# Performance work log

Hardware: AMD Instinct MI355X
Metric: run time of the kernel (lower is better)

## Reference

```python
import jax, jax.numpy as jnp
from jax import lax
import numpy as np

B, V, T, K, HE, TH, E, L = 128, 30000, 50, 50, 256, 800, 300, 3
DELTA = 0.005


def setup_inputs() -> dict:
    key = jax.random.key(0)
    ks = jax.random.split(key, 24)
    rn = lambda k, s, sc=0.05: jax.random.normal(k, s, jnp.float32) * sc
    return dict(
        X=jax.random.uniform(ks[0], (B, V), jnp.float32),
        timestamp=jax.random.randint(ks[1], (B,), 0, T),
        X_mean=jax.random.uniform(ks[2], (T, V), jnp.float32),
        W_eta_map=rn(ks[3], (HE, V)), b_eta_map=rn(ks[4], (HE,)),
        lstm_Wih=rn(ks[5], (L, 4 * HE, HE)), lstm_Whh=rn(ks[6], (L, 4 * HE, HE)),
        lstm_bih=rn(ks[7], (L, 4 * HE)), lstm_bhh=rn(ks[8], (L, 4 * HE)),
        W_qeta_mu=rn(ks[9], (K, HE + K)), b_qeta_mu=rn(ks[10], (K,)),
        W_qeta_ls=rn(ks[11], (K, HE + K)), b_qeta_ls=rn(ks[12], (K,)),
        W1=rn(ks[13], (TH, V + K)), b1=rn(ks[14], (TH,)),
        W2=rn(ks[15], (TH, TH)), b2=rn(ks[16], (TH,)),
        W_qt_mu=rn(ks[17], (K, TH)), b_qt_mu=rn(ks[18], (K,)),
        W_qt_ls=rn(ks[19], (K, TH)), b_qt_ls=rn(ks[20], (K,)),
        mu_q_alpha=rn(ks[21], (K, T, E), 0.1),
        logsigma_q_alpha=rn(ks[22], (K, T, E), 0.1),
        emb=rn(ks[23], (V, E), 0.1),
    )


def _lstm(x, Wih, Whh, bih, bhh):
    # PyTorch-style multi-layer LSTM, batch=1 squeezed away; x: [T, HE]
    for l in range(Wih.shape[0]):
        Wi, Wh, bi, bh = Wih[l], Whh[l], bih[l], bhh[l]
        def step(carry, xt, Wi=Wi, Wh=Wh, bi=bi, bh=bh):
            h, c = carry
            g = Wi @ xt + Wh @ h + bi + bh
            i, f, gg, o = jnp.split(g, 4)  # torch gate order i,f,g,o
            c = jax.nn.sigmoid(f) * c + jax.nn.sigmoid(i) * jnp.tanh(gg)
            h = jax.nn.sigmoid(o) * jnp.tanh(c)
            return (h, c), h
        H = Wh.shape[1]
        _, x = lax.scan(step, (jnp.zeros(H, x.dtype), jnp.zeros(H, x.dtype)), x)
    return x


def reference(X, timestamp, X_mean, W_eta_map, b_eta_map, lstm_Wih, lstm_Whh,
              lstm_bih, lstm_bhh, W_qeta_mu, b_qeta_mu, W_qeta_ls, b_qeta_ls,
              W1, b1, W2, b2, W_qt_mu, b_qt_mu, W_qt_ls, b_qt_ls,
              mu_q_alpha, logsigma_q_alpha, emb):
    # eval-mode DETM forward (reparameterize returns mu when not training)
    nb = X / X.sum(1, keepdims=True)
    logd = jnp.log(jnp.float32(DELTA))
    Tn = X_mean.shape[0]
    first = jnp.arange(Tn) == 0

    # --- eta: LSTM over time then sequential Gaussian recurrence ---
    rnn_out = _lstm(X_mean @ W_eta_map.T + b_eta_map, lstm_Wih, lstm_Whh, lstm_bih, lstm_bhh)  # [T,HE]
    Kn = W_qeta_mu.shape[0]

    def eta_step(eta_prev, xs):
        out_t, f = xs
        h = jnp.concatenate([out_t, eta_prev])
        mu = W_qeta_mu @ h + b_qeta_mu
        ls = W_qeta_ls @ h + b_qeta_ls
        p_ls = jnp.where(f, 0.0, logd)  # prior: N(0,I) at t=0, N(eta_{t-1}, delta) after
        kl = 0.5 * jnp.sum((jnp.exp(ls) + (mu - eta_prev) ** 2) / (jnp.exp(p_ls) + 1e-6) - 1.0 + p_ls - ls)
        return mu, (mu, kl)  # eval: eta_t = mu_t

    _, (etas, kls_eta) = lax.scan(eta_step, jnp.zeros(Kn, X.dtype), (rnn_out, first))
    kl_eta = kls_eta.sum()

    # --- theta ---
    eta_td = etas[timestamp]  # [B,K]
    h = jnp.tanh(jnp.concatenate([nb, eta_td], axis=1) @ W1.T + b1)
    h = jnp.tanh(h @ W2.T + b2)
    mu_t = h @ W_qt_mu.T + b_qt_mu
    ls_t = h @ W_qt_ls.T + b_qt_ls
    theta = jax.nn.softmax(mu_t, axis=-1)  # eval: z = mu
    kl_theta = (0.5 * jnp.sum((jnp.exp(ls_t) + (mu_t - eta_td) ** 2) / (1.0 + 1e-6) - 1.0 - ls_t, axis=-1)).sum()

    # --- alpha (eval: alpha_t = mu_q_alpha[:,t,:]) ---
    alphas = jnp.transpose(mu_q_alpha, (1, 0, 2))      # [T,K,E]
    q_ls = jnp.transpose(logsigma_q_alpha, (1, 0, 2))
    p_mu = jnp.concatenate([jnp.zeros_like(alphas[:1]), alphas[:-1]], axis=0)
    p_ls = jnp.where(first[:, None, None], 0.0, logd)
    kl_alpha = (0.5 * jnp.sum((jnp.exp(q_ls) + (alphas - p_mu) ** 2) / (jnp.exp(p_ls) + 1e-6) - 1.0 + p_ls - q_ls, axis=-1)).sum()

    # --- beta, likelihood ---
    beta = jax.nn.softmax(jnp.einsum('tke,ve->tkv', alphas, emb), axis=-1)  # [T,K,V]
    px = jnp.einsum('bk,bkv->bv', theta, beta[timestamp])
    lnpx = jnp.log(px + 1e-6)
    nll = (-lnpx * X).sum(-1).mean()
    return theta, lnpx, beta, nll, kl_alpha, kl_eta, kl_theta
```

## Files before the change

### kernel.cpp

```cpp
#include <hip/hip_runtime.h>
#include <math.h>

#define B_  128
#define V_  30000
#define T_  50
#define K_  50
#define HE_ 256
#define TH_ 800
#define E_  300
#define L_  3

#define LOGD_ (-5.2983173665480363f)

typedef short bf16x8 __attribute__((ext_vector_type(8)));
typedef float f32x4  __attribute__((ext_vector_type(4)));

#define TM 64
#define TN 64
#define TK 16

__global__ __launch_bounds__(256) void gemm_nt(
    const float* __restrict__ A, int lda, int M,
    const float* __restrict__ B, int ldb, int N,
    int K,
    float* __restrict__ C, int ldc,
    const float* __restrict__ bias, int mode, int kchunk)
{
    __shared__ float As[TK][TM + 4];
    __shared__ float Bs[TK][TN + 4];
    const int tid = threadIdx.x;
    const int bm = blockIdx.y * TM;
    const int bn = blockIdx.x * TN;
    const int tx = tid & 15;
    const int ty = tid >> 4;
    const int lr = tid >> 2;
    const int lc = (tid & 3) << 2;

    float acc[4][4];
#pragma unroll
    for (int i = 0; i < 4; ++i)
#pragma unroll
        for (int j = 0; j < 4; ++j) acc[i][j] = 0.f;

    const int kbeg = blockIdx.z * kchunk;
    const int kend = min(K, kbeg + kchunk);

    for (int k0 = kbeg; k0 < kend; k0 += TK) {
        {
            float v0 = 0.f, v1 = 0.f, v2 = 0.f, v3 = 0.f;
            int gr = bm + lr;
            if (gr < M) {
                const float* p = A + (size_t)gr * lda + k0 + lc;
                int rem = K - (k0 + lc);
                if (rem >= 4) {
                    float2 a0 = *(const float2*)p;
                    float2 a1 = *(const float2*)(p + 2);
                    v0 = a0.x; v1 = a0.y; v2 = a1.x; v3 = a1.y;
                } else {
                    if (rem > 0) v0 = p[0];
                    if (rem > 1) v1 = p[1];
                    if (rem > 2) v2 = p[2];
                }
            }
            As[lc + 0][lr] = v0; As[lc + 1][lr] = v1;
            As[lc + 2][lr] = v2; As[lc + 3][lr] = v3;
        }
        {
            float v0 = 0.f, v1 = 0.f, v2 = 0.f, v3 = 0.f;
            int gr = bn + lr;
            if (gr < N) {
                const float* p = B + (size_t)gr * ldb + k0 + lc;
                int rem = K - (k0 + lc);
                if (rem >= 4) {
                    float2 a0 = *(const float2*)p;
                    float2 a1 = *(const float2*)(p + 2);
                    v0 = a0.x; v1 = a0.y; v2 = a1.x; v3 = a1.y;
                } else {
                    if (rem > 0) v0 = p[0];
                    if (rem > 1) v1 = p[1];
                    if (rem > 2) v2 = p[2];
                }
            }
            Bs[lc + 0][lr] = v0; Bs[lc + 1][lr] = v1;
            Bs[lc + 2][lr] = v2; Bs[lc + 3][lr] = v3;
        }
        __syncthreads();
#pragma unroll
        for (int kk = 0; kk < TK; ++kk) {
            float a[4], b[4];
#pragma unroll
            for (int i = 0; i < 4; ++i) a[i] = As[kk][ty * 4 + i];
#pragma unroll
            for (int j = 0; j < 4; ++j) b[j] = Bs[kk][tx * 4 + j];
#pragma unroll
            for (int i = 0; i < 4; ++i)
#pragma unroll
                for (int j = 0; j < 4; ++j) acc[i][j] += a[i] * b[j];
        }
        __syncthreads();
    }

#pragma unroll
    for (int i = 0; i < 4; ++i) {
        int row = bm + ty * 4 + i;
        if (row >= M) continue;
#pragma unroll
        for (int j = 0; j < 4; ++j) {
            int col = bn + tx * 4 + j;
            if (col >= N) continue;
            float v = acc[i][j];
            if (mode == 3) {
                atomicAdd(&C[(size_t)row * ldc + col], v);
            } else {
                if (mode == 1) v = tanhf(v + bias[col]);
                else if (mode == 2) v = v + bias[col];
                C[(size_t)row * ldc + col] = v;
            }
        }
    }
}

__global__ __launch_bounds__(256) void bias_act(
    float* __restrict__ C, const float* __restrict__ bias,
    int total, int N, int mode)
{
    int idx = blockIdx.x * 256 + threadIdx.x;
    if (idx >= total) return;
    int j = idx % N;
    float v = C[idx] + bias[j];
    if (mode == 1) v = tanhf(v);
    C[idx] = v;
}

__global__ __launch_bounds__(256) void rowsum_inv(const float* __restrict__ X,
                                                  float* __restrict__ inv)
{
    int b = blockIdx.x;
    const float4* p = (const float4*)(X + (size_t)b * V_);
    float s = 0.f;
    for (int i = threadIdx.x; i < V_ / 4; i += 256) {
        float4 v = p[i];
        s += v.x + v.y + v.z + v.w;
    }
    for (int off = 32; off; off >>= 1) s += __shfl_down(s, off);
    __shared__ float red[4];
    int wid = threadIdx.x >> 6, lane = threadIdx.x & 63;
    if (lane == 0) red[wid] = s;
    __syncthreads();
    if (threadIdx.x == 0) inv[b] = 1.f / (red[0] + red[1] + red[2] + red[3]);
}

#define NLB 32

__global__ __launch_bounds__(256) void lstm_all(
    const float* __restrict__ rnn_in,
    const float* __restrict__ Wih,
    const float* __restrict__ Whh,
    const float* __restrict__ bih,
    const float* __restrict__ bhh,
    float* __restrict__ houtA,
    float* __restrict__ houtB,
    float* __restrict__ houtF,
    float* __restrict__ hping,
    int* __restrict__ barcnt)
{
    __shared__ float sx[8 * 36];
    __shared__ float sh[8 * 36];
    __shared__ float sg[32];
    const int tid = threadIdx.x;
    const int blk = blockIdx.x;
    const int row_local = tid >> 3;
    const int chunk = tid & 7;
    const int gate = row_local >> 3;
    const int jloc = row_local & 7;
    const int gr = gate * HE_ + blk * 8 + jloc;
    const int seg = tid >> 5, sidx = tid & 31;

    for (int l = 0; l < L_; ++l) {
        float4 wih[8], whh[8];
        const float4* pi = (const float4*)(Wih + ((size_t)l * 4 * HE_ + gr) * HE_ + chunk * 32);
        const float4* pw = (const float4*)(Whh + ((size_t)l * 4 * HE_ + gr) * HE_ + chunk * 32);
#pragma unroll
        for (int q = 0; q < 8; ++q) { wih[q] = pi[q]; whh[q] = pw[q]; }
        const float bias = bih[l * 4 * HE_ + gr] + bhh[l * 4 * HE_ + gr];
        const float* xs = (l == 0) ? rnn_in : ((l == 1) ? houtA : houtB);
        float* hd = (l == 0) ? houtA : ((l == 1) ? houtB : houtF);
        float cst = 0.f;

        for (int t = 0; t < T_; ++t) {
            const int wb = t & 1, rb = wb ^ 1;
            float xv = xs[t * HE_ + tid];
            float hv = (t > 0) ? hping[rb * HE_ + tid] : 0.f;
            sx[seg * 36 + sidx] = xv;
            sh[seg * 36 + sidx] = hv;
            __syncthreads();

            float acc = 0.f;
#pragma unroll
            for (int q = 0; q < 8; ++q) {
                float4 a = *(const float4*)&sx[chunk * 36 + q * 4];
                float4 b = *(const float4*)&sh[chunk * 36 + q * 4];
                float4 wa = wih[q], wc = whh[q];
                acc += wa.x * a.x + wa.y * a.y + wa.z * a.z + wa.w * a.w
                     + wc.x * b.x + wc.y * b.y + wc.z * b.z + wc.w * b.w;
            }
            acc += __shfl_xor(acc, 1);
            acc += __shfl_xor(acc, 2);
            acc += __shfl_xor(acc, 4);
            if (chunk == 0) sg[row_local] = acc + bias;
            __syncthreads();

            if (tid < 8) {
                float gi = sg[tid], gf = sg[8 + tid], gg = sg[16 + tid], go = sg[24 + tid];
                float si = 1.f / (1.f + expf(-gi));
                float sf = 1.f / (1.f + expf(-gf));
                float so = 1.f / (1.f + expf(-go));
                cst = sf * cst + si * tanhf(gg);
                float hn = so * tanhf(cst);
                int j = blk * 8 + tid;
                hping[wb * HE_ + j] = hn;
                hd[t * HE_ + j] = hn;
            }

            if (tid < 64) __threadfence();
            __syncthreads();
            if (tid == 0) {
                __hip_atomic_fetch_add(barcnt, 1, __ATOMIC_ACQ_REL, __HIP_MEMORY_SCOPE_AGENT);
                const int tgt = (l * T_ + t + 1) * NLB;
                while (__hip_atomic_load(barcnt, __ATOMIC_ACQUIRE, __HIP_MEMORY_SCOPE_AGENT) < tgt)
                    __builtin_amdgcn_s_sleep(1);
            }
            __syncthreads();
        }
    }
}

__global__ __launch_bounds__(256) void eta_scan(
    const float* __restrict__ rnn_out,
    const float* __restrict__ Wmu, const float* __restrict__ bmu,
    const float* __restrict__ Wls, const float* __restrict__ bls,
    float* __restrict__ etas,
    float* __restrict__ kl_eta_out)
{
    __shared__ float hbuf[HE_ + K_];
    __shared__ float smu[K_];
    __shared__ float red[256];
    const int tid = threadIdx.x;
    const int k = tid >> 2, c = tid & 3;
    if (tid < K_) hbuf[HE_ + tid] = 0.f;
    float kl = 0.f;
    __syncthreads();
    for (int t = 0; t < T_; ++t) {
        if (tid < HE_) hbuf[tid] = rnn_out[t * HE_ + tid];
        __syncthreads();
        if (k < K_) {
            const float* wm = Wmu + k * (HE_ + K_);
            const float* wl = Wls + k * (HE_ + K_);
            float am = 0.f, al = 0.f;
            for (int i = c; i < HE_ + K_; i += 4) {
                float hv = hbuf[i];
                am += wm[i] * hv;
                al += wl[i] * hv;
            }
            am += __shfl_xor(am, 1); am += __shfl_xor(am, 2);
            al += __shfl_xor(al, 1); al += __shfl_xor(al, 2);
            if (c == 0) {
                float mu = am + bmu[k];
                float ls = al + bls[k];
                float eprev = hbuf[HE_ + k];
                float pls = (t == 0) ? 0.f : LOGD_;
                float d = mu - eprev;
                kl += 0.5f * ((expf(ls) + d * d) / (expf(pls) + 1e-6f) - 1.f + pls - ls);
                etas[t * K_ + k] = mu;
                smu[k] = mu;
            }
        }
        __syncthreads();
        if (tid < K_) hbuf[HE_ + tid] = smu[tid];
        __syncthreads();
    }
    red[tid] = kl;
    __syncthreads();
    if (tid == 0) {
        float s = 0.f;
        for (int i = 0; i < 256; ++i) s += red[i];
        *kl_eta_out = s;
    }
}

__global__ __launch_bounds__(256) void h1_epilogue(
    const float* __restrict__ C1, const float* __restrict__ inv,
    const float* __restrict__ etas, const int* __restrict__ ts,
    const float* __restrict__ W1, const float* __restrict__ b1,
    float* __restrict__ h1)
{
    int idx = blockIdx.x * 256 + threadIdx.x;
    if (idx >= B_ * TH_) return;
    int b = idx / TH_, j = idx % TH_;
    const float* e = etas + ts[b] * K_;
    const float* w = W1 + (size_t)j * (V_ + K_) + V_;
    float s = 0.f;
#pragma unroll
    for (int k = 0; k < K_; ++k) s += e[k] * w[k];
    h1[idx] = tanhf(C1[idx] * inv[b] + s + b1[j]);
}

__global__ __launch_bounds__(64) void theta_kernel(
    const float* __restrict__ mu_t, const float* __restrict__ ls_t,
    const float* __restrict__ etas, const int* __restrict__ ts,
    float* __restrict__ theta, float* __restrict__ kl_out)
{
    int b = blockIdx.x;
    int lane = threadIdx.x;
    bool ok = lane < K_;
    float m = ok ? mu_t[b * K_ + lane] : -3.4e38f;
    float mx = m;
    for (int off = 32; off; off >>= 1) mx = fmaxf(mx, __shfl_down(mx, off));
    mx = __shfl(mx, 0);
    float e = ok ? expf(m - mx) : 0.f;
    float s = e;
    for (int off = 32; off; off >>= 1) s += __shfl_down(s, off);
    s = __shfl(s, 0);
    if (ok) theta[b * K_ + lane] = e / s;
    float kl = 0.f;
    if (ok) {
        float ls = ls_t[b * K_ + lane];
        float d = m - etas[ts[b] * K_ + lane];
        kl = 0.5f * ((expf(ls) + d * d) / (1.f + 1e-6f) - 1.f - ls);
    }
    for (int off = 32; off; off >>= 1) kl += __shfl_down(kl, off);
    if (lane == 0) atomicAdd(kl_out, kl);
}

#define KP_   320
#define MPAD_ 2560
#define NPAD_ 30080

__global__ __launch_bounds__(256) void conv_alpha(
    const float* __restrict__ mu, short* __restrict__ Ah, short* __restrict__ Al)
{
    int idx = blockIdx.x * 256 + threadIdx.x;
    if (idx >= MPAD_ * KP_) return;
    int row = idx / KP_, e = idx % KP_;
    float v = 0.f;
    if (row < T_ * K_ && e < E_) {
        int t = row / K_, k = row % K_;
        v = mu[((size_t)k * T_ + t) * E_ + e];
    }
    unsigned int u = __float_as_uint(v);
    Ah[idx] = (short)(u >> 16);
    float hf = __uint_as_float(u & 0xFFFF0000u);
    Al[idx] = (short)(__float_as_uint(v - hf) >> 16);
}

__global__ __launch_bounds__(512, 4) void gemm_beta(
    const short* __restrict__ Ah, const short* __restrict__ Al,
    const float* __restrict__ Bf,
    float* __restrict__ Cexp,
    float* __restrict__ bsum)
{
    __shared__ __align__(16) short lds[4 * 8192];
    const int tid = threadIdx.x;
    const int lane = tid & 63;
    const int w = tid >> 6;
    const int wr = w >> 2, wc = w & 3;
    const int l15 = lane & 15, l4 = lane >> 4;

    const int NM = MPAD_ / 128;
    const int nwg = (NPAD_ / 128) * NM;
    const int qq_ = nwg / 8, rr_ = nwg % 8;
    int orig = blockIdx.x;
    int xcd = orig & 7, ixc = orig >> 3;
    int wg = (xcd < rr_ ? xcd * (qq_ + 1) : rr_ * (qq_ + 1) + (xcd - rr_) * qq_) + ixc;
    const int bn = (wg / NM) * 128;
    const int bm = (wg % NM) * 128;

    f32x4 acc[4][2];
#pragma unroll
    for (int mi = 0; mi < 4; ++mi)
#pragma unroll
        for (int ni = 0; ni < 2; ++ni) acc[mi][ni] = (f32x4){0.f, 0.f, 0.f, 0.f};

    uint4  va[4];
    float4 vb[4];

    auto loadTile = [&](int k0) {
#pragma unroll
        for (int q = 0; q < 4; ++q) {
            int L = q * 512 + tid;
            int tile = L >> 10;
            int c = L & 1023;
            int r = c >> 3;
            int k8 = (c & 7) ^ (r & 7);
            const short* src = (tile ? Al : Ah) + (size_t)(bm + r) * KP_ + k0 + k8 * 8;
            va[q] = *(const uint4*)src;
        }
#pragma unroll
        for (int q = 0; q < 2; ++q) {
            int L = q * 512 + tid;
            int r = L >> 3;
            int k8 = (L & 7) ^ (r & 7);
            int rg = bn + r;
            int kb = k0 + k8 * 8;
            float4 u0, u1;
            if (rg < V_ && kb + 8 <= E_) {
                u0 = *(const float4*)(Bf + (size_t)rg * E_ + kb);
                u1 = *(const float4*)(Bf + (size_t)rg * E_ + kb + 4);
            } else {
                float t[8];
#pragma unroll
                for (int e = 0; e < 8; ++e) {
                    int kk = kb + e;
                    t[e] = (rg < V_ && kk < E_) ? Bf[(size_t)rg * E_ + kk] : 0.f;
                }
                u0.x = t[0]; u0.y = t[1]; u0.z = t[2]; u0.w = t[3];
                u1.x = t[4]; u1.y = t[5]; u1.z = t[6]; u1.w = t[7];
            }
            vb[q * 2] = u0; vb[q * 2 + 1] = u1;
        }
    };
    auto writeTile = [&]() {
#pragma unroll
        for (int q = 0; q < 4; ++q) {
            int L = q * 512 + tid;
            int tile = L >> 10;
            int c = L & 1023;
            *(uint4*)&lds[(size_t)(tile * 1024 + c) * 8] = va[q];
        }
#pragma unroll
        for (int q = 0; q < 2; ++q) {
            int L = q * 512 + tid;
            float vv[8];
            float4 u0 = vb[q * 2], u1 = vb[q * 2 + 1];
            vv[0] = u0.x; vv[1] = u0.y; vv[2] = u0.z; vv[3] = u0.w;
            vv[4] = u1.x; vv[5] = u1.y; vv[6] = u1.z; vv[7] = u1.w;
            unsigned int hpk[4], lpk[4];
#pragma unroll
            for (int e = 0; e < 8; e += 2) {
                unsigned int b0 = __float_as_uint(vv[e]);
                unsigned int b1 = __float_as_uint(vv[e + 1]);
                hpk[e >> 1] = (b0 >> 16) | (b1 & 0xFFFF0000u);
                float d0 = vv[e]     - __uint_as_float(b0 & 0xFFFF0000u);
                float d1 = vv[e + 1] - __uint_as_float(b1 & 0xFFFF0000u);
                lpk[e >> 1] = (__float_as_uint(d0) >> 16) | (__float_as_uint(d1) & 0xFFFF0000u);
            }
            uint4 hv; hv.x = hpk[0]; hv.y = hpk[1]; hv.z = hpk[2]; hv.w = hpk[3];
            uint4 lv; lv.x = lpk[0]; lv.y = lpk[1]; lv.z = lpk[2]; lv.w = lpk[3];
            *(uint4*)&lds[(size_t)(2048 + L) * 8] = hv;
            *(uint4*)&lds[(size_t)(3072 + L) * 8] = lv;
        }
    };

    loadTile(0);
    writeTile();
    __syncthreads();

    for (int k0 = 0; k0 < KP_; k0 += 64) {
        const bool nxt = (k0 + 64) < KP_;
        if (nxt) loadTile(k0 + 64);

#pragma unroll
        for (int ks = 0; ks < 2; ++ks) {
            bf16x8 fbh[2], fbl[2];
#pragma unroll
            for (int ni = 0; ni < 2; ++ni) {
                int r = wc * 32 + ni * 16 + l15;
                int s = r * 8 + ((ks * 4 + l4) ^ (r & 7));
                fbh[ni] = *(const bf16x8*)&lds[(size_t)(2048 + s) * 8];
                fbl[ni] = *(const bf16x8*)&lds[(size_t)(3072 + s) * 8];
            }
#pragma unroll
            for (int mi = 0; mi < 4; ++mi) {
                int r = wr * 64 + mi * 16 + l15;
                int s = r * 8 + ((ks * 4 + l4) ^ (r & 7));
                bf16x8 fah = *(const bf16x8*)&lds[(size_t)s * 8];
                bf16x8 fal = *(const bf16x8*)&lds[(size_t)(1024 + s) * 8];
#pragma unroll
                for (int ni = 0; ni < 2; ++ni) {
                    acc[mi][ni] = __builtin_amdgcn_mfma_f32_16x16x32_bf16(
                        fah, fbh[ni], acc[mi][ni], 0, 0, 0);
                    acc[mi][ni] = __builtin_amdgcn_mfma_f32_16x16x32_bf16(
                        fah, fbl[ni], acc[mi][ni], 0, 0, 0);
                    acc[mi][ni] = __builtin_amdgcn_mfma_f32_16x16x32_bf16(
                        fal, fbh[ni], acc[mi][ni], 0, 0, 0);
                }
            }
        }
        __syncthreads();
        if (nxt) {
            writeTile();
            __syncthreads();
        }
    }

#pragma unroll
    for (int mi = 0; mi < 4; ++mi) {
#pragma unroll
        for (int reg = 0; reg < 4; ++reg) {
            int grow = bm + wr * 64 + mi * 16 + (l4 << 2) + reg;
            float rs = 0.f;
            float ex[2];
#pragma unroll
            for (int ni = 0; ni < 2; ++ni) {
                int gcol = bn + wc * 32 + ni * 16 + l15;
                float e = (gcol < V_) ? __expf(acc[mi][ni][reg]) : 0.f;
                ex[ni] = e;
                rs += e;
            }
            if (grow < T_ * K_) {
#pragma unroll
                for (int ni = 0; ni < 2; ++ni) {
                    int gcol = bn + wc * 32 + ni * 16 + l15;
                    if (gcol < V_) Cexp[(size_t)grow * V_ + gcol] = ex[ni];
                }
            }
            rs += __shfl_xor(rs, 1);
            rs += __shfl_xor(rs, 2);
            rs += __shfl_xor(rs, 4);
            rs += __shfl_xor(rs, 8);
            if (l15 == 0 && grow < T_ * K_) atomicAdd(&bsum[grow], rs);
        }
    }
}

__global__ __launch_bounds__(256) void beta_scale(
    float* __restrict__ beta, const float* __restrict__ bsum)
{
    const int total4 = T_ * K_ * (V_ / 4);
    for (int i = blockIdx.x * 256 + threadIdx.x; i < total4; i += gridDim.x * 256) {
        int row = i / (V_ / 4);
        float inv = 1.f / bsum[row];
        float4 v = ((const float4*)beta)[i];
        v.x *= inv; v.y *= inv; v.z *= inv; v.w *= inv;
        ((float4*)beta)[i] = v;
    }
}

__global__ __launch_bounds__(256) void px_kernel(
    const float* __restrict__ beta, const float* __restrict__ theta,
    const int* __restrict__ ts, const float* __restrict__ X,
    float* __restrict__ lnpx, float* __restrict__ nll_acc)
{
    __shared__ float sb[K_][256];
    int t = blockIdx.y;
    int tid = threadIdx.x;
    int v = blockIdx.x * 256 + tid;
    bool vok = v < V_;
    bool any = false;
    for (int b = 0; b < B_; ++b) any |= (ts[b] == t);
    if (!any) return;
    for (int k = 0; k < K_; ++k)
        sb[k][tid] = vok ? beta[((size_t)t * K_ + k) * V_ + v] : 0.f;
    __syncthreads();
    float acc = 0.f;
    for (int b = 0; b < B_; ++b) {
        if (ts[b] != t) continue;
        const float* th = theta + b * K_;
        float px = 0.f;
#pragma unroll
        for (int k = 0; k < K_; ++k) px += th[k] * sb[k][tid];
        float l = logf(px + 1e-6f);
        if (vok) {
            lnpx[(size_t)b * V_ + v] = l;
            acc += l * X[(size_t)b * V_ + v];
        }
    }
    for (int off = 32; off; off >>= 1) acc += __shfl_down(acc, off);
    __shared__ float red[4];
    int wid = tid >> 6, lane = tid & 63;
    if (lane == 0) red[wid] = acc;
    __syncthreads();
    if (tid == 0) atomicAdd(nll_acc, red[0] + red[1] + red[2] + red[3]);
}

__global__ __launch_bounds__(256) void kl_alpha_kernel(
    const float* __restrict__ mu, const float* __restrict__ lsig,
    float* __restrict__ out)
{
    int idx = blockIdx.x * 256 + threadIdx.x;
    float term = 0.f;
    if (idx < K_ * T_ * E_) {
        int r = idx % (T_ * E_);
        int t = r / E_;
        float a = mu[idx];
        float q = lsig[idx];
        float pmu = (t > 0) ? mu[idx - E_] : 0.f;
        float pls = (t > 0) ? LOGD_ : 0.f;
        float d = a - pmu;
        term = 0.5f * ((expf(q) + d * d) / (expf(pls) + 1e-6f) - 1.f + pls - q);
    }
    for (int off = 32; off; off >>= 1) term += __shfl_down(term, off);
    __shared__ float red[4];
    int wid = threadIdx.x >> 6, lane = threadIdx.x & 63;
    if (lane == 0) red[wid] = term;
    __syncthreads();
    if (threadIdx.x == 0) atomicAdd(out, red[0] + red[1] + red[2] + red[3]);
}

__global__ void finalize_nll(const float* __restrict__ acc, float* __restrict__ out)
{
    *out = -acc[0] * (1.f / (float)B_);
}

extern "C" void kernel_launch(void* const* d_in, const int* in_sizes, int n_in,
                              void* d_out, int out_size, void* d_ws, size_t ws_size,
                              hipStream_t stream)
{
    const float* X          = (const float*)d_in[0];
    const int*   ts         = (const int*)d_in[1];
    const float* X_mean     = (const float*)d_in[2];
    const float* W_eta_map  = (const float*)d_in[3];
    const float* b_eta_map  = (const float*)d_in[4];
    const float* lstm_Wih   = (const float*)d_in[5];
    const float* lstm_Whh   = (const float*)d_in[6];
    const float* lstm_bih   = (const float*)d_in[7];
    const float* lstm_bhh   = (const float*)d_in[8];
    const float* W_qeta_mu  = (const float*)d_in[9];
    const float* b_qeta_mu  = (const float*)d_in[10];
    const float* W_qeta_ls  = (const float*)d_in[11];
    const float* b_qeta_ls  = (const float*)d_in[12];
    const float* W1         = (const float*)d_in[13];
    const float* b1         = (const float*)d_in[14];
    const float* W2         = (const float*)d_in[15];
    const float* b2         = (const float*)d_in[16];
    const float* W_qt_mu    = (const float*)d_in[17];
    const float* b_qt_mu    = (const float*)d_in[18];
    const float* W_qt_ls    = (const float*)d_in[19];
    const float* b_qt_ls    = (const float*)d_in[20];
    const float* mu_q_alpha = (const float*)d_in[21];
    const float* ls_q_alpha = (const float*)d_in[22];
    const float* emb        = (const float*)d_in[23];

    float* out     = (float*)d_out;
    float* o_theta = out;
    float* o_lnpx  = out + (size_t)B_ * K_;
    float* o_beta  = o_lnpx + (size_t)B_ * V_;
    float* o_scal  = o_beta + (size_t)T_ * K_ * V_;

    float* ws = (float*)d_ws;
    float* w_inv   = ws;
    float* w_rnn   = ws + 128;
    float* w_seq0  = ws + 12928;
    float* w_houtA = ws + 38528;
    float* w_houtB = ws + 51328;
    float* w_hping = ws + 64128;
    float* w_barc  = ws + 64640;
    float* w_etas  = ws + 89728;
    float* w_h1    = ws + 92228;
    float* w_h2    = ws + 194628;
    float* w_mu    = ws + 297028;
    float* w_ls    = ws + 303428;
    float* w_nll   = ws + 309828;
    float* w_bsum  = ws + 309832;
    short* w_Ah    = (short*)(ws + 312344);
    short* w_Al    = (short*)(ws + 721944);

    hipMemsetAsync(o_scal, 0, 4 * sizeof(float), stream);
    hipMemsetAsync(w_h1, 0, (size_t)(102400 + 102400 + 6400 + 6400 + 1) * sizeof(float), stream);
    hipMemsetAsync(w_rnn, 0, (size_t)T_ * HE_ * sizeof(float), stream);
    hipMemsetAsync(w_barc, 0, sizeof(int), stream);
    hipMemsetAsync(w_bsum, 0, (size_t)T_ * K_ * sizeof(float), stream);

    rowsum_inv<<<B_, 256, 0, stream>>>(X, w_inv);

    gemm_nt<<<dim3(HE_ / TN, 1, 125), 256, 0, stream>>>(
        X_mean, V_, T_, W_eta_map, V_, HE_, V_, w_rnn, HE_, nullptr, 3, 240);
    bias_act<<<(T_ * HE_ + 255) / 256, 256, 0, stream>>>(
        w_rnn, b_eta_map, T_ * HE_, HE_, 2);

    lstm_all<<<NLB, 256, 0, stream>>>(
        w_rnn, lstm_Wih, lstm_Whh, lstm_bih, lstm_bhh,
        w_houtA, w_houtB, w_seq0, w_hping, (int*)w_barc);

    eta_scan<<<1, 256, 0, stream>>>(w_seq0, W_qeta_mu, b_qeta_mu,
                                    W_qeta_ls, b_qeta_ls, w_etas, o_scal + 2);

    gemm_nt<<<dim3((TH_ + TN - 1) / TN, (B_ + TM - 1) / TM, 75), 256, 0, stream>>>(
        X, V_, B_, W1, V_ + K_, TH_, V_, w_h1, TH_, nullptr, 3, 400);
    h1_epilogue<<<(B_ * TH_ + 255) / 256, 256, 0, stream>>>(
        w_h1, w_inv, w_etas, ts, W1, b1, w_h1);

    gemm_nt<<<dim3((TH_ + TN - 1) / TN, (B_ + TM - 1) / TM, 10), 256, 0, stream>>>(
        w_h1, TH_, B_, W2, TH_, TH_, TH_, w_h2, TH_, nullptr, 3, 80);
    bias_act<<<(B_ * TH_ + 255) / 256, 256, 0, stream>>>(
        w_h2, b2, B_ * TH_, TH_, 1);

    gemm_nt<<<dim3(1, (B_ + TM - 1) / TM, 25), 256, 0, stream>>>(
        w_h2, TH_, B_, W_qt_mu, TH_, K_, TH_, w_mu, K_, nullptr, 3, 32);
    gemm_nt<<<dim3(1, (B_ + TM - 1) / TM, 25), 256, 0, stream>>>(
        w_h2, TH_, B_, W_qt_ls, TH_, K_, TH_, w_ls, K_, nullptr, 3, 32);
    bias_act<<<(B_ * K_ + 255) / 256, 256, 0, stream>>>(
        w_mu, b_qt_mu, B_ * K_, K_, 2);
    bias_act<<<(B_ * K_ + 255) / 256, 256, 0, stream>>>(
        w_ls, b_qt_ls, B_ * K_, K_, 2);

    theta_kernel<<<B_, 64, 0, stream>>>(w_mu, w_ls, w_etas, ts, o_theta, o_scal + 3);

    conv_alpha<<<(MPAD_ * KP_ + 255) / 256, 256, 0, stream>>>(mu_q_alpha, w_Ah, w_Al);
    gemm_beta<<<(NPAD_ / 128) * (MPAD_ / 128), 512, 0, stream>>>(
        w_Ah, w_Al, emb, o_beta, w_bsum);
    beta_scale<<<2048, 256, 0, stream>>>(o_beta, w_bsum);

    px_kernel<<<dim3((V_ + 255) / 256, T_), 256, 0, stream>>>(
        o_beta, o_theta, ts, X, o_lnpx, w_nll);

    kl_alpha_kernel<<<(K_ * T_ * E_ + 255) / 256, 256, 0, stream>>>(
        mu_q_alpha, ls_q_alpha, o_scal + 1);

    finalize_nll<<<1, 1, 0, stream>>>(w_nll, o_scal);
}
```

Baseline: 2.572 ms.

## Use split-bf16 MFMA GEMM for large reductions and pipeline LSTM layers

Adds a bf16x3 MFMA GEMM that splits each fp32 operand into high and low bf16 parts, with a swizzled LDS layout and register prefetch. It replaces the scalar fp32 GEMM for the two large V-length reductions (X_mean·W_eta and X·W1). The LSTM is restructured so each of the three layers runs on its own 16-block group, pipelined over time through per-layer counters instead of one global barrier per step. The trade-offs are slightly lower precision from the 3-term bf16 approximation and reliance on all 48 blocks being co-resident for the spin waits.

```diff
diff --git a/kernel.cpp b/kernel.cpp
--- a/kernel.cpp
+++ b/kernel.cpp
@@ -120,6 +120,144 @@
     }
 }
 
+__global__ __launch_bounds__(512, 4) void gemm_bf3(
+    const float* __restrict__ A, int lda, int M,
+    const float* __restrict__ B, int ldb, int N,
+    int K,
+    float* __restrict__ C, int ldc, int kchunk)
+{
+    __shared__ __align__(16) short lds[4 * 8192];
+    const int tid = threadIdx.x;
+    const int lane = tid & 63;
+    const int w = tid >> 6;
+    const int wr = w >> 2, wc = w & 3;
+    const int l15 = lane & 15, l4 = lane >> 4;
+    const int bm = blockIdx.y * 128;
+    const int bn = blockIdx.x * 128;
+    const int kbeg = blockIdx.z * kchunk;
+    const int kend = kbeg + kchunk;
+
+    f32x4 acc[4][2];
+#pragma unroll
+    for (int mi = 0; mi < 4; ++mi)
+#pragma unroll
+        for (int ni = 0; ni < 2; ++ni) acc[mi][ni] = (f32x4){0.f, 0.f, 0.f, 0.f};
+
+    float4 va[4], vb[4];
+
+    auto loadSide = [&](const float* __restrict__ P, int ldp, int Rlim,
+                        int base, int k0, float4* dst) {
+#pragma unroll
+        for (int q = 0; q < 2; ++q) {
+            int L = q * 512 + tid;
+            int r = L >> 3;
+            int k8 = (L & 7) ^ (r & 7);
+            int rg = base + r;
+            int kb = k0 + k8 * 8;
+            float4 u0, u1;
+            if (rg < Rlim && kb + 8 <= K) {
+                u0 = *(const float4*)(P + (size_t)rg * ldp + kb);
+                u1 = *(const float4*)(P + (size_t)rg * ldp + kb + 4);
+            } else {
+                float tt[8];
+#pragma unroll
+                for (int e = 0; e < 8; ++e) {
+                    int kk = kb + e;
+                    tt[e] = (rg < Rlim && kk < K) ? P[(size_t)rg * ldp + kk] : 0.f;
+                }
+                u0.x = tt[0]; u0.y = tt[1]; u0.z = tt[2]; u0.w = tt[3];
+                u1.x = tt[4]; u1.y = tt[5]; u1.z = tt[6]; u1.w = tt[7];
+            }
+            dst[q * 2] = u0; dst[q * 2 + 1] = u1;
+        }
+    };
+    auto writeSide = [&](const float4* src, int tbase) {
+#pragma unroll
+        for (int q = 0; q < 2; ++q) {
+            int L = q * 512 + tid;
+            float vv[8];
+            float4 u0 = src[q * 2], u1 = src[q * 2 + 1];
+            vv[0] = u0.x; vv[1] = u0.y; vv[2] = u0.z; vv[3] = u0.w;
+            vv[4] = u1.x; vv[5] = u1.y; vv[6] = u1.z; vv[7] = u1.w;
+            unsigned int hpk[4], lpk[4];
+#pragma unroll
+            for (int e = 0; e < 8; e += 2) {
+                unsigned int b0 = __float_as_uint(vv[e]);
+                unsigned int b1 = __float_as_uint(vv[e + 1]);
+                hpk[e >> 1] = (b0 >> 16) | (b1 & 0xFFFF0000u);
+                float d0 = vv[e]     - __uint_as_float(b0 & 0xFFFF0000u);
+                float d1 = vv[e + 1] - __uint_as_float(b1 & 0xFFFF0000u);
+                lpk[e >> 1] = (__float_as_uint(d0) >> 16) | (__float_as_uint(d1) & 0xFFFF0000u);
+            }
+            uint4 hv; hv.x = hpk[0]; hv.y = hpk[1]; hv.z = hpk[2]; hv.w = hpk[3];
+            uint4 lv; lv.x = lpk[0]; lv.y = lpk[1]; lv.z = lpk[2]; lv.w = lpk[3];
+            *(uint4*)&lds[(size_t)(tbase + L) * 8] = hv;
+            *(uint4*)&lds[(size_t)(tbase + 1024 + L) * 8] = lv;
+        }
+    };
+
+    loadSide(A, lda, M, bm, kbeg, va);
+    loadSide(B, ldb, N, bn, kbeg, vb);
+    writeSide(va, 0);
+    writeSide(vb, 2048);
+    __syncthreads();
+
+    for (int k0 = kbeg; k0 < kend; k0 += 64) {
+        const bool nxt = (k0 + 64) < kend;
+        if (nxt) {
+            loadSide(A, lda, M, bm, k0 + 64, va);
+            loadSide(B, ldb, N, bn, k0 + 64, vb);
+        }
+#pragma unroll
+        for (int ks = 0; ks < 2; ++ks) {
+            bf16x8 fbh[2], fbl[2];
+#pragma unroll
+            for (int ni = 0; ni < 2; ++ni) {
+                int r = wc * 32 + ni * 16 + l15;
+                int s = r * 8 + ((ks * 4 + l4) ^ (r & 7));
+                fbh[ni] = *(const bf16x8*)&lds[(size_t)(2048 + s) * 8];
+                fbl[ni] = *(const bf16x8*)&lds[(size_t)(3072 + s) * 8];
+            }
+#pragma unroll
+            for (int mi = 0; mi < 4; ++mi) {
+                int r = wr * 64 + mi * 16 + l15;
+                int s = r * 8 + ((ks * 4 + l4) ^ (r & 7));
+                bf16x8 fah = *(const bf16x8*)&lds[(size_t)s * 8];
+                bf16x8 fal = *(const bf16x8*)&lds[(size_t)(1024 + s) * 8];
+#pragma unroll
+                for (int ni = 0; ni < 2; ++ni) {
+                    acc[mi][ni] = __builtin_amdgcn_mfma_f32_16x16x32_bf16(
+                        fah, fbh[ni], acc[mi][ni], 0, 0, 0);
+                    acc[mi][ni] = __builtin_amdgcn_mfma_f32_16x16x32_bf16(
+                        fah, fbl[ni], acc[mi][ni], 0, 0, 0);
+                    acc[mi][ni] = __builtin_amdgcn_mfma_f32_16x16x32_bf16(
+                        fal, fbh[ni], acc[mi][ni], 0, 0, 0);
+                }
+            }
+        }
+        __syncthreads();
+        if (nxt) {
+            writeSide(va, 0);
+            writeSide(vb, 2048);
+            __syncthreads();
+        }
+    }
+
+#pragma unroll
+    for (int mi = 0; mi < 4; ++mi) {
+#pragma unroll
+        for (int reg = 0; reg < 4; ++reg) {
+            int grow = bm + wr * 64 + mi * 16 + (l4 << 2) + reg;
+            if (grow >= M) continue;
+#pragma unroll
+            for (int ni = 0; ni < 2; ++ni) {
+                int gcol = bn + wc * 32 + ni * 16 + l15;
+                if (gcol < N) atomicAdd(&C[(size_t)grow * ldc + gcol], acc[mi][ni][reg]);
+            }
+        }
+    }
+}
+
 __global__ __launch_bounds__(256) void bias_act(
     float* __restrict__ C, const float* __restrict__ bias,
     int total, int N, int mode)
@@ -150,9 +288,9 @@
     if (threadIdx.x == 0) inv[b] = 1.f / (red[0] + red[1] + red[2] + red[3]);
 }
 
-#define NLB 32
-
-__global__ __launch_bounds__(256) void lstm_all(
+#define GLB 16
+
+__global__ __launch_bounds__(256, 1) void lstm_pipe(
     const float* __restrict__ rnn_in,
     const float* __restrict__ Wih,
     const float* __restrict__ Whh,
@@ -161,77 +299,81 @@
     float* __restrict__ houtA,
     float* __restrict__ houtB,
     float* __restrict__ houtF,
-    float* __restrict__ hping,
-    int* __restrict__ barcnt)
-{
-    __shared__ float sx[8 * 36];
-    __shared__ float sh[8 * 36];
-    __shared__ float sg[32];
+    int* __restrict__ cnts)
+{
+    __shared__ __align__(16) float sx[HE_];
+    __shared__ __align__(16) float sh[HE_];
+    __shared__ float sg[64];
     const int tid = threadIdx.x;
-    const int blk = blockIdx.x;
-    const int row_local = tid >> 3;
-    const int chunk = tid & 7;
-    const int gate = row_local >> 3;
-    const int jloc = row_local & 7;
-    const int gr = gate * HE_ + blk * 8 + jloc;
-    const int seg = tid >> 5, sidx = tid & 31;
-
-    for (int l = 0; l < L_; ++l) {
-        float4 wih[8], whh[8];
-        const float4* pi = (const float4*)(Wih + ((size_t)l * 4 * HE_ + gr) * HE_ + chunk * 32);
-        const float4* pw = (const float4*)(Whh + ((size_t)l * 4 * HE_ + gr) * HE_ + chunk * 32);
-#pragma unroll
-        for (int q = 0; q < 8; ++q) { wih[q] = pi[q]; whh[q] = pw[q]; }
-        const float bias = bih[l * 4 * HE_ + gr] + bhh[l * 4 * HE_ + gr];
-        const float* xs = (l == 0) ? rnn_in : ((l == 1) ? houtA : houtB);
-        float* hd = (l == 0) ? houtA : ((l == 1) ? houtB : houtF);
-        float cst = 0.f;
-
-        for (int t = 0; t < T_; ++t) {
-            const int wb = t & 1, rb = wb ^ 1;
-            float xv = xs[t * HE_ + tid];
-            float hv = (t > 0) ? hping[rb * HE_ + tid] : 0.f;
-            sx[seg * 36 + sidx] = xv;
-            sh[seg * 36 + sidx] = hv;
-            __syncthreads();
-
-            float acc = 0.f;
-#pragma unroll
-            for (int q = 0; q < 8; ++q) {
-                float4 a = *(const float4*)&sx[chunk * 36 + q * 4];
-                float4 b = *(const float4*)&sh[chunk * 36 + q * 4];
-                float4 wa = wih[q], wc = whh[q];
-                acc += wa.x * a.x + wa.y * a.y + wa.z * a.z + wa.w * a.w
-                     + wc.x * b.x + wc.y * b.y + wc.z * b.z + wc.w * b.w;
-            }
-            acc += __shfl_xor(acc, 1);
-            acc += __shfl_xor(acc, 2);
-            acc += __shfl_xor(acc, 4);
-            if (chunk == 0) sg[row_local] = acc + bias;
-            __syncthreads();
-
-            if (tid < 8) {
-                float gi = sg[tid], gf = sg[8 + tid], gg = sg[16 + tid], go = sg[24 + tid];
-                float si = 1.f / (1.f + expf(-gi));
-                float sf = 1.f / (1.f + expf(-gf));
-                float so = 1.f / (1.f + expf(-go));
-                cst = sf * cst + si * tanhf(gg);
-                float hn = so * tanhf(cst);
-                int j = blk * 8 + tid;
-                hping[wb * HE_ + j] = hn;
-                hd[t * HE_ + j] = hn;
-            }
-
-            if (tid < 64) __threadfence();
-            __syncthreads();
-            if (tid == 0) {
-                __hip_atomic_fetch_add(barcnt, 1, __ATOMIC_ACQ_REL, __HIP_MEMORY_SCOPE_AGENT);
-                const int tgt = (l * T_ + t + 1) * NLB;
-                while (__hip_atomic_load(barcnt, __ATOMIC_ACQUIRE, __HIP_MEMORY_SCOPE_AGENT) < tgt)
+    const int l   = blockIdx.x / GLB;
+    const int blk = blockIdx.x % GLB;
+    const int row_local = tid >> 2;
+    const int chunk = tid & 3;
+    const int gate = row_local >> 4;
+    const int jloc = row_local & 15;
+    const int gr = gate * HE_ + blk * 16 + jloc;
+
+    float4 wih[16], whh[16];
+    const float4* pi = (const float4*)(Wih + ((size_t)l * 4 * HE_ + gr) * HE_ + chunk * 64);
+    const float4* pw = (const float4*)(Whh + ((size_t)l * 4 * HE_ + gr) * HE_ + chunk * 64);
+#pragma unroll
+    for (int q = 0; q < 16; ++q) { wih[q] = pi[q]; whh[q] = pw[q]; }
+    const float bias = bih[l * 4 * HE_ + gr] + bhh[l * 4 * HE_ + gr];
+
+    const float* xs = (l == 0) ? rnn_in : ((l == 1) ? houtA : houtB);
+    float* hd = (l == 0) ? houtA : ((l == 1) ? houtB : houtF);
+    int* cin  = cnts + (l - 1) * 32;
+    int* cown = cnts + l * 32;
+
+    float cst = 0.f;
+    for (int t = 0; t < T_; ++t) {
+        if (tid == 0) {
+            if (l > 0) {
+                const int tgt = (t + 1) * GLB;
+                while (__hip_atomic_load(cin, __ATOMIC_ACQUIRE, __HIP_MEMORY_SCOPE_AGENT) < tgt)
                     __builtin_amdgcn_s_sleep(1);
             }
-            __syncthreads();
-        }
+            if (t > 0) {
+                const int tgt = t * GLB;
+                while (__hip_atomic_load(cown, __ATOMIC_ACQUIRE, __HIP_MEMORY_SCOPE_AGENT) < tgt)
+                    __builtin_amdgcn_s_sleep(1);
+            }
+        }
+        __syncthreads();
+
+        sx[tid] = xs[t * HE_ + tid];
+        sh[tid] = (t > 0) ? hd[(t - 1) * HE_ + tid] : 0.f;
+        __syncthreads();
+
+        float acc = 0.f;
+        const float4* xa = (const float4*)&sx[chunk * 64];
+        const float4* ha = (const float4*)&sh[chunk * 64];
+#pragma unroll
+        for (int q = 0; q < 16; ++q) {
+            float4 a = xa[q], b = ha[q];
+            float4 wa = wih[q], wc = whh[q];
+            acc += wa.x * a.x + wa.y * a.y + wa.z * a.z + wa.w * a.w
+                 + wc.x * b.x + wc.y * b.y + wc.z * b.z + wc.w * b.w;
+        }
+        acc += __shfl_xor(acc, 1);
+        acc += __shfl_xor(acc, 2);
+        if (chunk == 0) sg[row_local] = acc + bias;
+        __syncthreads();
+
+        if (tid < 16) {
+            float gi = sg[tid], gf = sg[16 + tid], gg = sg[32 + tid], go = sg[48 + tid];
+            float si = 1.f / (1.f + expf(-gi));
+            float sf = 1.f / (1.f + expf(-gf));
+            float so = 1.f / (1.f + expf(-go));
+            cst = sf * cst + si * tanhf(gg);
+            float hn = so * tanhf(cst);
+            hd[t * HE_ + blk * 16 + tid] = hn;
+        }
+        if (tid == 0) {
+            __threadfence();
+            __hip_atomic_fetch_add(cown, 1, __ATOMIC_RELEASE, __HIP_MEMORY_SCOPE_AGENT);
+        }
+        __syncthreads();
     }
 }
 
@@ -643,8 +785,7 @@
     float* w_seq0  = ws + 12928;
     float* w_houtA = ws + 38528;
     float* w_houtB = ws + 51328;
-    float* w_hping = ws + 64128;
-    float* w_barc  = ws + 64640;
+    float* w_cnt   = ws + 64640;
     float* w_etas  = ws + 89728;
     float* w_h1    = ws + 92228;
     float* w_h2    = ws + 194628;
@@ -658,25 +799,25 @@
     hipMemsetAsync(o_scal, 0, 4 * sizeof(float), stream);
     hipMemsetAsync(w_h1, 0, (size_t)(102400 + 102400 + 6400 + 6400 + 1) * sizeof(float), stream);
     hipMemsetAsync(w_rnn, 0, (size_t)T_ * HE_ * sizeof(float), stream);
-    hipMemsetAsync(w_barc, 0, sizeof(int), stream);
+    hipMemsetAsync(w_cnt, 0, 96 * sizeof(int), stream);
     hipMemsetAsync(w_bsum, 0, (size_t)T_ * K_ * sizeof(float), stream);
 
     rowsum_inv<<<B_, 256, 0, stream>>>(X, w_inv);
 
-    gemm_nt<<<dim3(HE_ / TN, 1, 125), 256, 0, stream>>>(
-        X_mean, V_, T_, W_eta_map, V_, HE_, V_, w_rnn, HE_, nullptr, 3, 240);
+    gemm_bf3<<<dim3(2, 1, 47), 512, 0, stream>>>(
+        X_mean, V_, T_, W_eta_map, V_, HE_, V_, w_rnn, HE_, 640);
     bias_act<<<(T_ * HE_ + 255) / 256, 256, 0, stream>>>(
         w_rnn, b_eta_map, T_ * HE_, HE_, 2);
 
-    lstm_all<<<NLB, 256, 0, stream>>>(
+    lstm_pipe<<<3 * GLB, 256, 0, stream>>>(
         w_rnn, lstm_Wih, lstm_Whh, lstm_bih, lstm_bhh,
-        w_houtA, w_houtB, w_seq0, w_hping, (int*)w_barc);
+        w_houtA, w_houtB, w_seq0, (int*)w_cnt);
 
     eta_scan<<<1, 256, 0, stream>>>(w_seq0, W_qeta_mu, b_qeta_mu,
                                     W_qeta_ls, b_qeta_ls, w_etas, o_scal + 2);
 
-    gemm_nt<<<dim3((TH_ + TN - 1) / TN, (B_ + TM - 1) / TM, 75), 256, 0, stream>>>(
-        X, V_, B_, W1, V_ + K_, TH_, V_, w_h1, TH_, nullptr, 3, 400);
+    gemm_bf3<<<dim3((TH_ + 127) / 128, 1, 10), 512, 0, stream>>>(
+        X, V_, B_, W1, V_ + K_, TH_, V_, w_h1, TH_, 3008);
     h1_epilogue<<<(B_ * TH_ + 255) / 256, 256, 0, stream>>>(
         w_h1, w_inv, w_etas, ts, W1, b1, w_h1);
 
```

Result: faster. 2.239 ms (-13.0%).
